# Performance work log

Hardware: AMD Instinct MI355X
Metric: run time of the kernel (lower is better)

Reference implementation:

```python
import jax, jax.numpy as jnp
import numpy as np

ALPHA = 0.2  # LeakyReLU negative slope
NEG_INF = -9e15


def gat_layer(h_in, adj_mask, W, a, concat):
    """Classic pyGAT dense GraphAttentionLayer (eval mode, dropout=identity).
    h_in: [B, N, Fin], adj_mask: [N, N] bool, W: [Fin, Fout], a: [2*Fout, 1].
    """
    h = jnp.einsum('bnf,fo->bno', h_in, W)          # [B, N, Fout]
    Fo = W.shape[1]
    f1 = h @ a[:Fo, 0]                               # [B, N] scores for source
    f2 = h @ a[Fo:, 0]                               # [B, N] scores for target
    e = jax.nn.leaky_relu(f1[:, :, None] + f2[:, None, :], negative_slope=ALPHA)
    e = jnp.where(adj_mask[None, :, :], e, NEG_INF)  # mask non-edges
    attn = jax.nn.softmax(e, axis=-1)                # normalize over neighbors
    out = jnp.einsum('bij,bjo->bio', attn, h)        # weighted aggregation
    return jax.nn.elu(out) if concat else out


def setup_inputs() -> dict:
    key = jax.random.key(0)
    ks = jax.random.split(key, 7)
    B, T, N = 2, 17, 1024
    nfeat, nhid, nclass, nheads = 64, 64, 64, 4
    x = jax.random.normal(ks[0], (B, T, N, nfeat), dtype=jnp.float32)
    adj = jax.random.randint(ks[1], (N, N), 0, 2, dtype=jnp.int32)
    W_heads = jax.random.normal(ks[2], (nheads, nfeat, nhid), dtype=jnp.float32) / np.sqrt(nfeat)
    a_heads = jax.random.normal(ks[3], (nheads, 2 * nhid, 1), dtype=jnp.float32) / np.sqrt(2 * nhid)
    W_out = jax.random.normal(ks[4], (nhid * nheads, nclass), dtype=jnp.float32) / np.sqrt(nhid * nheads)
    a_out = jax.random.normal(ks[5], (2 * nclass, 1), dtype=jnp.float32) / np.sqrt(2 * nclass)
    return {"x": x, "adj": adj, "W_heads": W_heads, "a_heads": a_heads,
            "W_out": W_out, "a_out": a_out, "pred_step": 1}


def reference(x, adj, W_heads, a_heads, W_out, a_out, pred_step):
    B, T, N, F = x.shape
    Tp = T - pred_step
    mask = adj > 0
    # All time steps are independent -> fold (B, Tp) into one batch axis.
    xt = x[:, :Tp].reshape(B * Tp, N, F)
    nheads = W_heads.shape[0]
    heads = [gat_layer(xt, mask, W_heads[h], a_heads[h], concat=True)
             for h in range(nheads)]
    hcat = jnp.concatenate(heads, axis=-1)           # [B*Tp, N, nhid*nheads]
    out = jax.nn.relu(gat_layer(hcat, mask, W_out, a_out, concat=False))
    return out.reshape(B, Tp, N, -1)
```

## Files before the change

kernel.cpp:

```cpp
#include <hip/hip_runtime.h>
#include <hip/hip_bf16.h>

typedef short bf16x8 __attribute__((ext_vector_type(8)));
typedef float f32x4 __attribute__((ext_vector_type(4)));
typedef _Float16 half8 __attribute__((ext_vector_type(8)));
typedef _Float16 half4 __attribute__((ext_vector_type(4)));
typedef __fp16 cvt2_t __attribute__((ext_vector_type(2)));

#define N_NODES 1024
#define FDIM 64
#define NG 32
#define LOG2E 1.44269504088896f

__global__ __launch_bounds__(256) void k_prep(const int* __restrict__ adj,
                                              const float* __restrict__ Wh,
                                              const float* __restrict__ Wo,
                                              unsigned char* __restrict__ Mbyte,
                                              _Float16* __restrict__ wt1,
                                              _Float16* __restrict__ wt2) {
    const int bb = blockIdx.x, t = threadIdx.x;
    if (bb < 128) {
        int w = bb * 256 + t;
        const int* p = adj + (size_t)w * 32;
        unsigned r[8];
#pragma unroll
        for (int q = 0; q < 8; q++) {
            int4 a = ((const int4*)p)[q];
            r[q] = (a.x > 0 ? 1u : 0u) | (a.y > 0 ? 1u << 8 : 0u) |
                   (a.z > 0 ? 1u << 16 : 0u) | (a.w > 0 ? 1u << 24 : 0u);
        }
        uint4* dst = (uint4*)(Mbyte + (size_t)w * 32);
        dst[0] = (uint4){r[0], r[1], r[2], r[3]};
        dst[1] = (uint4){r[4], r[5], r[6], r[7]};
    } else if (bb < 132) {
        const int row = (bb - 128) * 64 + (t >> 2);
        const int kq = t & 3;
        const float* src = Wh + (size_t)(row >> 6) * 4096 + (row & 63);
#pragma unroll
        for (int kk = 0; kk < 16; kk += 8) {
            const int k0 = kq * 16 + kk;
            union { half8 v; cvt2_t c[4]; } pk_;
#pragma unroll
            for (int j = 0; j < 8; j += 2)
                pk_.c[j >> 1] = __builtin_amdgcn_cvt_pkrtz(src[(k0 + j) * 64],
                                                           src[(k0 + j + 1) * 64]);
            *(half8*)(wt1 + (size_t)row * 64 + k0) = pk_.v;
        }
    } else {
        const int o = (bb - 132) * 16 + (t >> 4);
        const int k0 = (t & 15) * 16;
        const float* src = Wo + o;
#pragma unroll
        for (int kk = 0; kk < 16; kk += 8) {
            union { half8 v; cvt2_t c[4]; } pk_;
#pragma unroll
            for (int j = 0; j < 8; j += 2)
                pk_.c[j >> 1] = __builtin_amdgcn_cvt_pkrtz(src[(k0 + kk + j) * 64],
                                                           src[(k0 + kk + j + 1) * 64]);
            *(half8*)(wt2 + (size_t)o * 256 + k0 + kk) = pk_.v;
        }
    }
}

__global__ __launch_bounds__(512, 2) void k_proj1(const float* __restrict__ x,
                                                  const _Float16* __restrict__ wt1,
                                                  const float* __restrict__ ah,
                                                  _Float16* __restrict__ H1T,
                                                  float* __restrict__ F1,
                                                  float* __restrict__ F2) {
    __shared__ _Float16 xs[128][64];
    const int t = threadIdx.x;
    const int nb = blockIdx.x, g = blockIdx.y;
    const int n0 = nb * 128;
    const int b = g >> 4, tstep = g & 15;

    {
        const int r = t >> 2, cq = t & 3;
        const float* xr = x + (((size_t)(b * 17 + tstep) * N_NODES + n0 + r) * FDIM) + cq * 16;
        float4 v0 = *(const float4*)(xr);
        float4 v1 = *(const float4*)(xr + 4);
        float4 v2 = *(const float4*)(xr + 8);
        float4 v3 = *(const float4*)(xr + 12);
        union { half8 v; cvt2_t c[4]; } u0, u1;
        u0.c[0] = __builtin_amdgcn_cvt_pkrtz(v0.x, v0.y);
        u0.c[1] = __builtin_amdgcn_cvt_pkrtz(v0.z, v0.w);
        u0.c[2] = __builtin_amdgcn_cvt_pkrtz(v1.x, v1.y);
        u0.c[3] = __builtin_amdgcn_cvt_pkrtz(v1.z, v1.w);
        u1.c[0] = __builtin_amdgcn_cvt_pkrtz(v2.x, v2.y);
        u1.c[1] = __builtin_amdgcn_cvt_pkrtz(v2.z, v2.w);
        u1.c[2] = __builtin_amdgcn_cvt_pkrtz(v3.x, v3.y);
        u1.c[3] = __builtin_amdgcn_cvt_pkrtz(v3.z, v3.w);
        *(half8*)&xs[r][((2 * cq) ^ (r & 7)) * 8] = u0.v;
        *(half8*)&xs[r][((2 * cq + 1) ^ (r & 7)) * 8] = u1.v;
    }
    __syncthreads();

    const int wv = t >> 6, ln = t & 63, li = ln & 15, grp = ln >> 4;
    const int arow = wv * 16 + li;

    f32x4 acc[16];
#pragma unroll
    for (int q = 0; q < 16; q++) acc[q] = (f32x4){0.f, 0.f, 0.f, 0.f};

#pragma unroll
    for (int s = 0; s < 2; s++) {
        half8 af = *(const half8*)&xs[arow][((s * 4 + grp) ^ (arow & 7)) * 8];
#pragma unroll
        for (int tile = 0; tile < 16; tile++) {
            half8 bf = *(const half8*)(wt1 + (size_t)(tile * 16 + li) * 64 + s * 32 + grp * 8);
            acc[tile] = __builtin_amdgcn_mfma_f32_16x16x32_f16(af, bf, acc[tile], 0, 0, 0);
        }
    }

    const int nbase = n0 + wv * 16 + grp * 4;
#pragma unroll
    for (int h = 0; h < 4; h++) {
        float p1[4] = {0.f, 0.f, 0.f, 0.f}, p2[4] = {0.f, 0.f, 0.f, 0.f};
#pragma unroll
        for (int ot = 0; ot < 4; ot++) {
            float a1v = ah[h * 128 + ot * 16 + li];
            float a2v = ah[h * 128 + 64 + ot * 16 + li];
            f32x4 A = acc[h * 4 + ot];
#pragma unroll
            for (int r = 0; r < 4; r++) {
                p1[r] = fmaf(A[r], a1v, p1[r]);
                p2[r] = fmaf(A[r], a2v, p2[r]);
            }
        }
#pragma unroll
        for (int m = 1; m < 16; m <<= 1)
#pragma unroll
            for (int r = 0; r < 4; r++) {
                p1[r] += __shfl_xor(p1[r], m);
                p2[r] += __shfl_xor(p2[r], m);
            }
        if (li == 0) {
            const size_t gh = (size_t)h * NG + g;
#pragma unroll
            for (int r = 0; r < 4; r++) {
                F1[gh * N_NODES + nbase + r] = p1[r] * LOG2E;
                F2[gh * N_NODES + nbase + r] = p2[r] * LOG2E;
            }
        }
    }
#pragma unroll
    for (int tile = 0; tile < 16; tile++) {
        const int h = tile >> 2, ot = tile & 3;
        union { half4 v; cvt2_t c[2]; } st;
        st.c[0] = __builtin_amdgcn_cvt_pkrtz(acc[tile][0], acc[tile][1]);
        st.c[1] = __builtin_amdgcn_cvt_pkrtz(acc[tile][2], acc[tile][3]);
        _Float16* dst = H1T + (((size_t)h * NG + g) * FDIM + ot * 16 + li) * N_NODES + nbase;
        *(half4*)dst = st.v;
    }
}

template<int CONCAT>
__global__ __launch_bounds__(512, 4) void k_attn(
    const _Float16* __restrict__ HT,
    const float* __restrict__ F1,
    const float* __restrict__ F2,
    const unsigned char* __restrict__ Mb,
    _Float16* __restrict__ HC,
    float* __restrict__ out)
{
    __shared__ _Float16 vt[2][64][256];
    __shared__ float f2s[N_NODES];
    const int t = threadIdx.x;
    const int g = blockIdx.x, h = blockIdx.y, nb = blockIdx.z;
    const int i0 = nb * 128;
    const size_t gidx = CONCAT ? ((size_t)h * NG + g) : (size_t)g;

    ((float2*)f2s)[t] = ((const float2*)(F2 + gidx * N_NODES))[t];

    const int wv = t >> 6, ln = t & 63;
    const int li = ln & 15, grp = ln >> 4, jb = grp * 8;
    const int lx = li & 7;
    const int il = wv * 16 + li;
    const float f1v = F1[gidx * N_NODES + i0 + il];

    const _Float16* Hg = HT + gidx * (size_t)(FDIM * N_NODES);
    const int srow = wv * 8 + (ln >> 3);
    const int swu = (ln & 7) ^ (srow & 7);
    const _Float16* srcb = Hg + (size_t)srow * N_NODES + (ln & 7) * 8;
    const unsigned char* Mrow = Mb + (size_t)(i0 + il) * N_NODES + jb;

    f32x4 acc[4], acc5;
#pragma unroll
    for (int q = 0; q < 4; q++) acc[q] = (f32x4){0.f, 0.f, 0.f, 0.f};
    acc5 = (f32x4){0.f, 0.f, 0.f, 0.f};

    union { half8 v; unsigned short s[8]; } onesu;
#pragma unroll
    for (int q = 0; q < 8; q++) onesu.s[q] = 0x3C00;
    const half8 ones = onesu.v;

    half8 stg[4];
    uint2 mbuf[2][8];
#pragma unroll
    for (int k2 = 0; k2 < 4; k2++) stg[k2] = *(const half8*)(srcb + k2 * 64);
#pragma unroll
    for (int k2 = 0; k2 < 4; k2++)
        *(half8*)&vt[0][srow][(k2 * 8 + swu) * 8] = stg[k2];
#pragma unroll
    for (int k2 = 0; k2 < 4; k2++) stg[k2] = *(const half8*)(srcb + 256 + k2 * 64);
#pragma unroll
    for (int q = 0; q < 8; q++) mbuf[0][q] = *(const uint2*)(Mrow + q * 32);
    __syncthreads();

    const float* f2p = &f2s[jb];
    float4 fa = *(const float4*)f2p;
    float4 fb = *(const float4*)(f2p + 4);

#pragma unroll
    for (int jt = 0; jt < 4; jt++) {
        if (jt < 3) {
#pragma unroll
            for (int k2 = 0; k2 < 4; k2++)
                *(half8*)&vt[(jt + 1) & 1][srow][(k2 * 8 + swu) * 8] = stg[k2];
#pragma unroll
            for (int q = 0; q < 8; q++)
                mbuf[(jt + 1) & 1][q] = *(const uint2*)(Mrow + (jt + 1) * 256 + q * 32);
        }
        if (jt < 2) {
#pragma unroll
            for (int k2 = 0; k2 < 4; k2++)
                stg[k2] = *(const half8*)(srcb + (jt + 2) * 256 + k2 * 64);
        }

#pragma unroll
        for (int jc = 0; jc < 8; jc++) {
            const uint2 w = mbuf[jt & 1][jc];
            const float4 cfa = fa, cfb = fb;
            if (!(jt == 3 && jc == 7)) {
                fa = *(const float4*)(f2p + 32);
                fb = *(const float4*)(f2p + 36);
            }
            f2p += 32;

            float b0 = (float)(unsigned char)(w.x);
            float b1 = (float)(unsigned char)(w.x >> 8);
            float b2 = (float)(unsigned char)(w.x >> 16);
            float b3 = (float)(w.x >> 24);
            float b4 = (float)(unsigned char)(w.y);
            float b5 = (float)(unsigned char)(w.y >> 8);
            float b6 = (float)(unsigned char)(w.y >> 16);
            float b7 = (float)(w.y >> 24);

            union { half8 v; cvt2_t c[4]; } afr;
            float s0, s1, p0, p1;
            s0 = f1v + cfa.x; s1 = f1v + cfa.y;
            s0 = fmaxf(s0, 0.2f * s0); s1 = fmaxf(s1, 0.2f * s1);
            p0 = __builtin_amdgcn_exp2f(s0) * b0;
            p1 = __builtin_amdgcn_exp2f(s1) * b1;
            afr.c[0] = __builtin_amdgcn_cvt_pkrtz(p0, p1);
            s0 = f1v + cfa.z; s1 = f1v + cfa.w;
            s0 = fmaxf(s0, 0.2f * s0); s1 = fmaxf(s1, 0.2f * s1);
            p0 = __builtin_amdgcn_exp2f(s0) * b2;
            p1 = __builtin_amdgcn_exp2f(s1) * b3;
            afr.c[1] = __builtin_amdgcn_cvt_pkrtz(p0, p1);
            s0 = f1v + cfb.x; s1 = f1v + cfb.y;
            s0 = fmaxf(s0, 0.2f * s0); s1 = fmaxf(s1, 0.2f * s1);
            p0 = __builtin_amdgcn_exp2f(s0) * b4;
            p1 = __builtin_amdgcn_exp2f(s1) * b5;
            afr.c[2] = __builtin_amdgcn_cvt_pkrtz(p0, p1);
            s0 = f1v + cfb.z; s1 = f1v + cfb.w;
            s0 = fmaxf(s0, 0.2f * s0); s1 = fmaxf(s1, 0.2f * s1);
            p0 = __builtin_amdgcn_exp2f(s0) * b6;
            p1 = __builtin_amdgcn_exp2f(s1) * b7;
            afr.c[3] = __builtin_amdgcn_cvt_pkrtz(p0, p1);

            const int ub = (jc >> 1) * 8 + (((jc & 1) * 4 + grp) ^ lx);
#pragma unroll
            for (int q = 0; q < 4; q++) {
                half8 bfr = *(const half8*)&vt[jt & 1][q * 16 + li][ub * 8];
                acc[q] = __builtin_amdgcn_mfma_f32_16x16x32_f16(afr.v, bfr, acc[q], 0, 0, 0);
            }
            acc5 = __builtin_amdgcn_mfma_f32_16x16x32_f16(afr.v, ones, acc5, 0, 0, 0);
        }
        if (jt < 3) __syncthreads();
    }

    float rin[4];
#pragma unroll
    for (int r2 = 0; r2 < 4; r2++) rin[r2] = 1.0f / acc5[r2];

    if (CONCAT) {
        _Float16* HCg = HC + (size_t)g * N_NODES * 256 + h * 64;
#pragma unroll
        for (int q = 0; q < 4; q++)
#pragma unroll
            for (int r2 = 0; r2 < 4; r2++) {
                int irow = wv * 16 + grp * 4 + r2;
                float v = acc[q][r2] * rin[r2];
                v = v > 0.f ? v : expm1f(v);
                HCg[(size_t)(i0 + irow) * 256 + q * 16 + li] = (_Float16)v;
            }
    } else {
        float* og = out + (size_t)g * N_NODES * FDIM;
#pragma unroll
        for (int q = 0; q < 4; q++)
#pragma unroll
            for (int r2 = 0; r2 < 4; r2++) {
                int irow = wv * 16 + grp * 4 + r2;
                float v = acc[q][r2] * rin[r2];
                og[(size_t)(i0 + irow) * FDIM + q * 16 + li] = v > 0.f ? v : 0.f;
            }
    }
}

__global__ __launch_bounds__(512, 2) void k_proj2(const _Float16* __restrict__ HC,
                                                  const _Float16* __restrict__ wt2,
                                                  const float* __restrict__ ao,
                                                  _Float16* __restrict__ H2T,
                                                  float* __restrict__ F1b,
                                                  float* __restrict__ F2b) {
    __shared__ _Float16 xs[128][256];
    const int t = threadIdx.x;
    const int nb = blockIdx.x, g = blockIdx.y;
    const int n0 = nb * 128;

    {
        const int r = t >> 2, cq = t & 3;
        const _Float16* src = HC + ((size_t)g * N_NODES + n0 + r) * 256 + cq * 64;
#pragma unroll
        for (int uu = 0; uu < 8; uu++) {
            int u = cq * 8 + uu;
            half8 v = *(const half8*)(src + uu * 8);
            int us = (u & 24) | ((u ^ r) & 7);
            *(half8*)&xs[r][us * 8] = v;
        }
    }
    __syncthreads();

    const int wv = t >> 6, ln = t & 63, li = ln & 15, grp = ln >> 4;
    const int arow = wv * 16 + li;

    f32x4 acc[4];
#pragma unroll
    for (int q = 0; q < 4; q++) acc[q] = (f32x4){0.f, 0.f, 0.f, 0.f};

#pragma unroll
    for (int s = 0; s < 8; s++) {
        int u = s * 4 + grp;
        int us = (u & 24) | ((u ^ arow) & 7);
        half8 af = *(const half8*)&xs[arow][us * 8];
#pragma unroll
        for (int tile = 0; tile < 4; tile++) {
            half8 bf = *(const half8*)(wt2 + (size_t)(tile * 16 + li) * 256 + s * 32 + grp * 8);
            acc[tile] = __builtin_amdgcn_mfma_f32_16x16x32_f16(af, bf, acc[tile], 0, 0, 0);
        }
    }

    const int nbase = n0 + wv * 16 + grp * 4;
    {
        float p1[4] = {0.f, 0.f, 0.f, 0.f}, p2[4] = {0.f, 0.f, 0.f, 0.f};
#pragma unroll
        for (int ot = 0; ot < 4; ot++) {
            float a1v = ao[ot * 16 + li];
            float a2v = ao[64 + ot * 16 + li];
            f32x4 A = acc[ot];
#pragma unroll
            for (int r = 0; r < 4; r++) {
                p1[r] = fmaf(A[r], a1v, p1[r]);
                p2[r] = fmaf(A[r], a2v, p2[r]);
            }
        }
#pragma unroll
        for (int m = 1; m < 16; m <<= 1)
#pragma unroll
            for (int r = 0; r < 4; r++) {
                p1[r] += __shfl_xor(p1[r], m);
                p2[r] += __shfl_xor(p2[r], m);
            }
        if (li == 0) {
#pragma unroll
            for (int r = 0; r < 4; r++) {
                F1b[(size_t)g * N_NODES + nbase + r] = p1[r] * LOG2E;
                F2b[(size_t)g * N_NODES + nbase + r] = p2[r] * LOG2E;
            }
        }
    }
#pragma unroll
    for (int tile = 0; tile < 4; tile++) {
        union { half4 v; cvt2_t c[2]; } st;
        st.c[0] = __builtin_amdgcn_cvt_pkrtz(acc[tile][0], acc[tile][1]);
        st.c[1] = __builtin_amdgcn_cvt_pkrtz(acc[tile][2], acc[tile][3]);
        _Float16* dst = H2T + ((size_t)g * FDIM + tile * 16 + li) * N_NODES + nbase;
        *(half4*)dst = st.v;
    }
}

extern "C" void kernel_launch(void* const* d_in, const int* in_sizes, int n_in,
                              void* d_out, int out_size, void* d_ws, size_t ws_size,
                              hipStream_t stream) {
    const float* x  = (const float*)d_in[0];
    const int* adj  = (const int*)d_in[1];
    const float* Wh = (const float*)d_in[2];
    const float* ah = (const float*)d_in[3];
    const float* Wo = (const float*)d_in[4];
    const float* ao = (const float*)d_in[5];

    char* ws = (char*)d_ws;
    unsigned char* Mbyte = (unsigned char*)(ws);
    _Float16* wt1 = (_Float16*)(ws + 1048576);
    _Float16* wt2 = (_Float16*)(ws + 1081344);
    float* F1  = (float*)(ws + 1114112);
    float* F2  = (float*)(ws + 1638400);
    float* F1b = (float*)(ws + 2162688);
    float* F2b = (float*)(ws + 2293760);
    _Float16* H1T = (_Float16*)(ws + 2424832);
    _Float16* HC  = (_Float16*)(ws + 2424832 + 16777216);
    _Float16* H2T = (_Float16*)(ws + 2424832 + 33554432);
    float* out = (float*)d_out;

    k_prep   <<<dim3(136),       dim3(256), 0, stream>>>(adj, Wh, Wo, Mbyte, wt1, wt2);
    k_proj1  <<<dim3(8, 32),     dim3(512), 0, stream>>>(x, wt1, ah, H1T, F1, F2);
    k_attn<1><<<dim3(32, 4, 8),  dim3(512), 0, stream>>>(H1T, F1, F2, Mbyte, HC, nullptr);
    k_proj2  <<<dim3(8, 32),     dim3(512), 0, stream>>>(HC, wt2, ao, H2T, F1b, F2b);
    k_attn<0><<<dim3(32, 1, 8),  dim3(512), 0, stream>>>(H2T, F1b, F2b, Mbyte, nullptr, out);
}
```

Before: 109.2 us.

## Factor leaky-relu exponentials into per-node terms and single-buffer the value tile

The inner loop no longer evaluates exp2(leakyrelu(f1+f2)) for every edge. The projection kernels precompute per-node exponentials, and the weight becomes max(exp(f2), K_i*exp(0.2 f2)) scaled by the mask, which removes the per-element transcendental. The attention kernel also moves from a double-buffered LDS value tile to a single buffer with two barriers per tile, and keeps two f2-derived arrays in LDS. Without a max-subtraction, the products of exponentials may overflow or lose precision in fp16, and the single buffer cuts load/compute overlap.

```diff
diff --git a/kernel.cpp b/kernel.cpp
--- a/kernel.cpp
+++ b/kernel.cpp
@@ -66,8 +66,9 @@
                                                   const _Float16* __restrict__ wt1,
                                                   const float* __restrict__ ah,
                                                   _Float16* __restrict__ H1T,
-                                                  float* __restrict__ F1,
-                                                  float* __restrict__ F2) {
+                                                  float* __restrict__ Kv,
+                                                  float* __restrict__ EB,
+                                                  float* __restrict__ ED) {
     __shared__ _Float16 xs[128][64];
     const int t = threadIdx.x;
     const int nb = blockIdx.x, g = blockIdx.y;
@@ -138,8 +139,10 @@
             const size_t gh = (size_t)h * NG + g;
 #pragma unroll
             for (int r = 0; r < 4; r++) {
-                F1[gh * N_NODES + nbase + r] = p1[r] * LOG2E;
-                F2[gh * N_NODES + nbase + r] = p2[r] * LOG2E;
+                float phi1 = p1[r] * LOG2E, phi2 = p2[r] * LOG2E;
+                Kv[gh * N_NODES + nbase + r] = __builtin_amdgcn_exp2f(-0.8f * phi1);
+                EB[gh * N_NODES + nbase + r] = __builtin_amdgcn_exp2f(phi2);
+                ED[gh * N_NODES + nbase + r] = __builtin_amdgcn_exp2f(0.2f * phi2);
             }
         }
     }
@@ -157,26 +160,29 @@
 template<int CONCAT>
 __global__ __launch_bounds__(512, 4) void k_attn(
     const _Float16* __restrict__ HT,
-    const float* __restrict__ F1,
-    const float* __restrict__ F2,
+    const float* __restrict__ Kv,
+    const float* __restrict__ EB,
+    const float* __restrict__ ED,
     const unsigned char* __restrict__ Mb,
     _Float16* __restrict__ HC,
     float* __restrict__ out)
 {
-    __shared__ _Float16 vt[2][64][256];
-    __shared__ float f2s[N_NODES];
+    __shared__ _Float16 vt[64][256];
+    __shared__ float ebs[N_NODES];
+    __shared__ float eds[N_NODES];
     const int t = threadIdx.x;
     const int g = blockIdx.x, h = blockIdx.y, nb = blockIdx.z;
     const int i0 = nb * 128;
     const size_t gidx = CONCAT ? ((size_t)h * NG + g) : (size_t)g;
 
-    ((float2*)f2s)[t] = ((const float2*)(F2 + gidx * N_NODES))[t];
+    ((float2*)ebs)[t] = ((const float2*)(EB + gidx * N_NODES))[t];
+    ((float2*)eds)[t] = ((const float2*)(ED + gidx * N_NODES))[t];
 
     const int wv = t >> 6, ln = t & 63;
     const int li = ln & 15, grp = ln >> 4, jb = grp * 8;
     const int lx = li & 7;
     const int il = wv * 16 + li;
-    const float f1v = F1[gidx * N_NODES + i0 + il];
+    const float kv_ = Kv[gidx * N_NODES + i0 + il];
 
     const _Float16* Hg = HT + gidx * (size_t)(FDIM * N_NODES);
     const int srow = wv * 8 + (ln >> 3);
@@ -199,43 +205,33 @@
 #pragma unroll
     for (int k2 = 0; k2 < 4; k2++) stg[k2] = *(const half8*)(srcb + k2 * 64);
 #pragma unroll
-    for (int k2 = 0; k2 < 4; k2++)
-        *(half8*)&vt[0][srow][(k2 * 8 + swu) * 8] = stg[k2];
-#pragma unroll
-    for (int k2 = 0; k2 < 4; k2++) stg[k2] = *(const half8*)(srcb + 256 + k2 * 64);
-#pragma unroll
     for (int q = 0; q < 8; q++) mbuf[0][q] = *(const uint2*)(Mrow + q * 32);
-    __syncthreads();
-
-    const float* f2p = &f2s[jb];
-    float4 fa = *(const float4*)f2p;
-    float4 fb = *(const float4*)(f2p + 4);
 
 #pragma unroll
     for (int jt = 0; jt < 4; jt++) {
+        __syncthreads();
+#pragma unroll
+        for (int k2 = 0; k2 < 4; k2++)
+            *(half8*)&vt[srow][(k2 * 8 + swu) * 8] = stg[k2];
         if (jt < 3) {
 #pragma unroll
             for (int k2 = 0; k2 < 4; k2++)
-                *(half8*)&vt[(jt + 1) & 1][srow][(k2 * 8 + swu) * 8] = stg[k2];
+                stg[k2] = *(const half8*)(srcb + (jt + 1) * 256 + k2 * 64);
 #pragma unroll
             for (int q = 0; q < 8; q++)
                 mbuf[(jt + 1) & 1][q] = *(const uint2*)(Mrow + (jt + 1) * 256 + q * 32);
         }
-        if (jt < 2) {
-#pragma unroll
-            for (int k2 = 0; k2 < 4; k2++)
-                stg[k2] = *(const half8*)(srcb + (jt + 2) * 256 + k2 * 64);
-        }
+        __syncthreads();
 
 #pragma unroll
         for (int jc = 0; jc < 8; jc++) {
             const uint2 w = mbuf[jt & 1][jc];
-            const float4 cfa = fa, cfb = fb;
-            if (!(jt == 3 && jc == 7)) {
-                fa = *(const float4*)(f2p + 32);
-                fb = *(const float4*)(f2p + 36);
-            }
-            f2p += 32;
+            const float* ebp = &ebs[jt * 256 + jc * 32 + jb];
+            const float* edp = &eds[jt * 256 + jc * 32 + jb];
+            float4 ea0 = *(const float4*)ebp;
+            float4 ea1 = *(const float4*)(ebp + 4);
+            float4 ec0 = *(const float4*)edp;
+            float4 ec1 = *(const float4*)(edp + 4);
 
             float b0 = (float)(unsigned char)(w.x);
             float b1 = (float)(unsigned char)(w.x >> 8);
@@ -246,38 +242,29 @@
             float b6 = (float)(unsigned char)(w.y >> 16);
             float b7 = (float)(w.y >> 24);
 
+            float q0 = fmaxf(ea0.x, kv_ * ec0.x) * b0;
+            float q1 = fmaxf(ea0.y, kv_ * ec0.y) * b1;
+            float q2 = fmaxf(ea0.z, kv_ * ec0.z) * b2;
+            float q3 = fmaxf(ea0.w, kv_ * ec0.w) * b3;
+            float q4 = fmaxf(ea1.x, kv_ * ec1.x) * b4;
+            float q5 = fmaxf(ea1.y, kv_ * ec1.y) * b5;
+            float q6 = fmaxf(ea1.z, kv_ * ec1.z) * b6;
+            float q7 = fmaxf(ea1.w, kv_ * ec1.w) * b7;
+
             union { half8 v; cvt2_t c[4]; } afr;
-            float s0, s1, p0, p1;
-            s0 = f1v + cfa.x; s1 = f1v + cfa.y;
-            s0 = fmaxf(s0, 0.2f * s0); s1 = fmaxf(s1, 0.2f * s1);
-            p0 = __builtin_amdgcn_exp2f(s0) * b0;
-            p1 = __builtin_amdgcn_exp2f(s1) * b1;
-            afr.c[0] = __builtin_amdgcn_cvt_pkrtz(p0, p1);
-            s0 = f1v + cfa.z; s1 = f1v + cfa.w;
-            s0 = fmaxf(s0, 0.2f * s0); s1 = fmaxf(s1, 0.2f * s1);
-            p0 = __builtin_amdgcn_exp2f(s0) * b2;
-            p1 = __builtin_amdgcn_exp2f(s1) * b3;
-            afr.c[1] = __builtin_amdgcn_cvt_pkrtz(p0, p1);
-            s0 = f1v + cfb.x; s1 = f1v + cfb.y;
-            s0 = fmaxf(s0, 0.2f * s0); s1 = fmaxf(s1, 0.2f * s1);
-            p0 = __builtin_amdgcn_exp2f(s0) * b4;
-            p1 = __builtin_amdgcn_exp2f(s1) * b5;
-            afr.c[2] = __builtin_amdgcn_cvt_pkrtz(p0, p1);
-            s0 = f1v + cfb.z; s1 = f1v + cfb.w;
-            s0 = fmaxf(s0, 0.2f * s0); s1 = fmaxf(s1, 0.2f * s1);
-            p0 = __builtin_amdgcn_exp2f(s0) * b6;
-            p1 = __builtin_amdgcn_exp2f(s1) * b7;
-            afr.c[3] = __builtin_amdgcn_cvt_pkrtz(p0, p1);
+            afr.c[0] = __builtin_amdgcn_cvt_pkrtz(q0, q1);
+            afr.c[1] = __builtin_amdgcn_cvt_pkrtz(q2, q3);
+            afr.c[2] = __builtin_amdgcn_cvt_pkrtz(q4, q5);
+            afr.c[3] = __builtin_amdgcn_cvt_pkrtz(q6, q7);
 
             const int ub = (jc >> 1) * 8 + (((jc & 1) * 4 + grp) ^ lx);
 #pragma unroll
             for (int q = 0; q < 4; q++) {
-                half8 bfr = *(const half8*)&vt[jt & 1][q * 16 + li][ub * 8];
+                half8 bfr = *(const half8*)&vt[q * 16 + li][ub * 8];
                 acc[q] = __builtin_amdgcn_mfma_f32_16x16x32_f16(afr.v, bfr, acc[q], 0, 0, 0);
             }
             acc5 = __builtin_amdgcn_mfma_f32_16x16x32_f16(afr.v, ones, acc5, 0, 0, 0);
         }
-        if (jt < 3) __syncthreads();
     }
 
     float rin[4];
@@ -312,8 +299,9 @@
                                                   const _Float16* __restrict__ wt2,
                                                   const float* __restrict__ ao,
                                                   _Float16* __restrict__ H2T,
-                                                  float* __restrict__ F1b,
-                                                  float* __restrict__ F2b) {
+                                                  float* __restrict__ Kv2,
+                                                  float* __restrict__ EB2,
+                                                  float* __restrict__ ED2) {
     __shared__ _Float16 xs[128][256];
     const int t = threadIdx.x;
     const int nb = blockIdx.x, g = blockIdx.y;
@@ -375,8 +363,10 @@
         if (li == 0) {
 #pragma unroll
             for (int r = 0; r < 4; r++) {
-                F1b[(size_t)g * N_NODES + nbase + r] = p1[r] * LOG2E;
-                F2b[(size_t)g * N_NODES + nbase + r] = p2[r] * LOG2E;
+                float phi1 = p1[r] * LOG2E, phi2 = p2[r] * LOG2E;
+                Kv2[(size_t)g * N_NODES + nbase + r] = __builtin_amdgcn_exp2f(-0.8f * phi1);
+                EB2[(size_t)g * N_NODES + nbase + r] = __builtin_amdgcn_exp2f(phi2);
+                ED2[(size_t)g * N_NODES + nbase + r] = __builtin_amdgcn_exp2f(0.2f * phi2);
             }
         }
     }
@@ -404,18 +394,20 @@
     unsigned char* Mbyte = (unsigned char*)(ws);
     _Float16* wt1 = (_Float16*)(ws + 1048576);
     _Float16* wt2 = (_Float16*)(ws + 1081344);
-    float* F1  = (float*)(ws + 1114112);
-    float* F2  = (float*)(ws + 1638400);
-    float* F1b = (float*)(ws + 2162688);
-    float* F2b = (float*)(ws + 2293760);
-    _Float16* H1T = (_Float16*)(ws + 2424832);
-    _Float16* HC  = (_Float16*)(ws + 2424832 + 16777216);
-    _Float16* H2T = (_Float16*)(ws + 2424832 + 33554432);
+    float* Kv1 = (float*)(ws + 1114112);
+    float* EB1 = (float*)(ws + 1638400);
+    float* ED1 = (float*)(ws + 2162688);
+    float* Kv2 = (float*)(ws + 2686976);
+    float* EB2 = (float*)(ws + 2818048);
+    float* ED2 = (float*)(ws + 2949120);
+    _Float16* H1T = (_Float16*)(ws + 3080192);
+    _Float16* HC  = (_Float16*)(ws + 3080192 + 16777216);
+    _Float16* H2T = (_Float16*)(ws + 3080192 + 33554432);
     float* out = (float*)d_out;
 
     k_prep   <<<dim3(136),       dim3(256), 0, stream>>>(adj, Wh, Wo, Mbyte, wt1, wt2);
-    k_proj1  <<<dim3(8, 32),     dim3(512), 0, stream>>>(x, wt1, ah, H1T, F1, F2);
-    k_attn<1><<<dim3(32, 4, 8),  dim3(512), 0, stream>>>(H1T, F1, F2, Mbyte, HC, nullptr);
-    k_proj2  <<<dim3(8, 32),     dim3(512), 0, stream>>>(HC, wt2, ao, H2T, F1b, F2b);
-    k_attn<0><<<dim3(32, 1, 8),  dim3(512), 0, stream>>>(H2T, F1b, F2b, Mbyte, nullptr, out);
+    k_proj1  <<<dim3(8, 32),     dim3(512), 0, stream>>>(x, wt1, ah, H1T, Kv1, EB1, ED1);
+    k_attn<1><<<dim3(32, 4, 8),  dim3(512), 0, stream>>>(H1T, Kv1, EB1, ED1, Mbyte, HC, nullptr);
+    k_proj2  <<<dim3(8, 32),     dim3(512), 0, stream>>>(HC, wt2, ao, H2T, Kv2, EB2, ED2);
+    k_attn<0><<<dim3(32, 1, 8),  dim3(512), 0, stream>>>(H2T, Kv2, EB2, ED2, Mbyte, nullptr, out);
 }
```

Result: slower. 114.2 us (+4.6%).
